# Kernel tuning notes

Measured on AMD Instinct MI355X. Metric: run time of the kernel, lower is better.

Reference implementation:

```python
import jax, jax.numpy as jnp
import numpy as np

B, N, F, K = 512, 512, 512, 10
D = F // 2

def setup_inputs() -> dict:
    key = jax.random.key(0)
    k1, k2, k3 = jax.random.split(key, 3)
    ins_emb = jax.random.normal(k1, (B, N, F), dtype=jnp.float32)
    attn = jax.random.uniform(k2, (B, N, 1), dtype=jnp.float32)
    # xavier_uniform for a (D, D) linear weight
    limit = float(np.sqrt(6.0 / (D + D)))
    W = jax.random.uniform(k3, (D, D), dtype=jnp.float32, minval=-limit, maxval=limit)
    return {"ins_emb": ins_emb, "attn": attn, "W": W}

def reference(ins_emb, attn, W):
    d = ins_emb.shape[-1] // 2
    drug = ins_emb[:, :, :d]          # [B, N, d]
    dis = ins_emb[:, :, d:]           # [B, N, d]
    # torch Linear: drug @ W^T, then per-instance dot with dis -> scalar
    proj = jnp.einsum('bnd,ed->bne', drug, W)          # [B, N, d]
    pred = jnp.sum(proj * dis, axis=-1, keepdims=True) # [B, N, 1]
    attn_pred = attn * pred                            # [B, N, 1]
    topk_vals, _ = jax.lax.top_k(attn_pred[:, :, 0], K)  # [B, K]
    return jnp.mean(topk_vals, axis=1, keepdims=True)    # [B, 1]
```

## Files before the change

### kernel.cpp

```cpp
#include <hip/hip_runtime.h>
#include <hip/hip_bf16.h>
#include <cstdint>

#define BB 512
#define NN 512
#define FF 512
#define DD 256
#define KTOP 10
#define BN (BB*NN)
#define BM 16
#define NTILES (BN/BM)
#define GRID 256
#define TPB (NTILES/GRID)

typedef __attribute__((ext_vector_type(8))) short bf16x8;
typedef __attribute__((ext_vector_type(4))) short s16x4;
typedef __attribute__((ext_vector_type(4))) float f32x4;

__device__ __forceinline__ ushort f2bf(float x){
  union { __hip_bfloat16 h; ushort u; } cv;
  cv.h = __float2bfloat16(x);
  return cv.u;
}

__device__ __forceinline__ bf16x8 cvt8(f32x4 a, f32x4 b){
  bf16x8 r;
  r[0]=(short)f2bf(a[0]); r[1]=(short)f2bf(a[1]); r[2]=(short)f2bf(a[2]); r[3]=(short)f2bf(a[3]);
  r[4]=(short)f2bf(b[0]); r[5]=(short)f2bf(b[1]); r[6]=(short)f2bf(b[2]); r[7]=(short)f2bf(b[3]);
  return r;
}

#define GL2LDS(GSRC, LDST)                                                          \
  __builtin_amdgcn_global_load_lds(                                                 \
      (const __attribute__((address_space(1))) uint32_t*)(uintptr_t)(GSRC),         \
      (__attribute__((address_space(3))) uint32_t*)(uint32_t)(uintptr_t)(LDST),     \
      16, 0, 0)

__global__ void wconv(const float* __restrict__ W, ushort* __restrict__ Wbf){
  int i = (blockIdx.x*256 + threadIdx.x)*4;
  float4 v = *reinterpret_cast<const float4*>(W + i);
  s16x4 o;
  o[0] = (short)f2bf(v.x); o[1] = (short)f2bf(v.y);
  o[2] = (short)f2bf(v.z); o[3] = (short)f2bf(v.w);
  *reinterpret_cast<s16x4*>(Wbf + i) = o;
}

__global__ __launch_bounds__(512, 2)
void score_kernel(const float* __restrict__ emb, const float* __restrict__ attn,
                  const ushort* __restrict__ Wbf, float* __restrict__ scores){
  __shared__ float Lbuf[4][BM*FF];
  __shared__ float red[2][8][BM];
  __shared__ float attn_l[TPB*BM];

  const int tid  = threadIdx.x;
  const int w    = tid >> 6;
  const int lane = tid & 63;
  const int g    = lane >> 4;
  const int c    = lane & 15;
  const int s    = w & 3;
  const int h    = w >> 2;

  attn_l[tid]       = attn[blockIdx.x*(TPB*BM) + tid];
  attn_l[tid + 512] = attn[blockIdx.x*(TPB*BM) + 512 + tid];

  bf16x8 Wf[4][4];
#pragma unroll
  for (int eb = 0; eb < 4; ++eb)
#pragma unroll
    for (int kb = 0; kb < 4; ++kb){
      int e = s*64 + eb*16 + c;
      int k = h*128 + kb*32 + g*8;
      Wf[eb][kb] = *reinterpret_cast<const bf16x8*>(Wbf + e*DD + k);
    }

  int offs[4];
#pragma unroll
  for (int i = 0; i < 4; ++i){
    int idx = w*4 + i;
    int r = idx >> 1, hf = idx & 1;
    offs[i] = r*FF + hf*256 + ((lane ^ (r & 7)) << 2);
  }
  const float* tbase = emb + (size_t)blockIdx.x * TPB * (BM*FF);

#pragma unroll
  for (int tt = 0; tt < 3; ++tt){
    const float* nb = tbase + (size_t)tt * (BM*FF);
#pragma unroll
    for (int i = 0; i < 4; ++i)
      GL2LDS(nb + offs[i], &Lbuf[tt][(w*4 + i)*256]);
  }

  for (int t = 0; t < TPB; ++t){
    if (t + 2 < TPB)      asm volatile("s_waitcnt vmcnt(8) lgkmcnt(0)" ::: "memory");
    else if (t + 1 < TPB) asm volatile("s_waitcnt vmcnt(4) lgkmcnt(0)" ::: "memory");
    else                  asm volatile("s_waitcnt vmcnt(0) lgkmcnt(0)" ::: "memory");
    __builtin_amdgcn_s_barrier();
    __builtin_amdgcn_sched_barrier(0);

    if (t + 3 < TPB){
      const float* nb = tbase + (size_t)(t+3) * (BM*FF);
#pragma unroll
      for (int i = 0; i < 4; ++i)
        GL2LDS(nb + offs[i], &Lbuf[(t+3) & 3][(w*4 + i)*256]);
    }

    if (t > 0 && tid < BM){
      const int tp = t - 1;
      float sum = red[tp&1][0][tid] + red[tp&1][1][tid] + red[tp&1][2][tid] + red[tp&1][3][tid]
                + red[tp&1][4][tid] + red[tp&1][5][tid] + red[tp&1][6][tid] + red[tp&1][7][tid];
      int row = (blockIdx.x*TPB + tp)*BM + tid;
      scores[row] = attn_l[tp*BM + tid] * sum;
    }

    const f32x4* Lv = (const f32x4*)&Lbuf[t & 3][0];
    const int rb = c*128;
    const int x  = c & 7;
    bf16x8 af[4];
#pragma unroll
    for (int kb = 0; kb < 4; ++kb){
      int ch0 = h*32 + kb*8 + g*2;
      f32x4 q0 = Lv[rb + ((ch0    ) ^ x)];
      f32x4 q1 = Lv[rb + ((ch0 + 1) ^ x)];
      af[kb] = cvt8(q0, q1);
    }
    float rs0=0.f, rs1=0.f, rs2=0.f, rs3=0.f;
#pragma unroll
    for (int eb = 0; eb < 4; ++eb){
      f32x4 acc = {0.f, 0.f, 0.f, 0.f};
#pragma unroll
      for (int kb = 0; kb < 4; ++kb)
        acc = __builtin_amdgcn_mfma_f32_16x16x32_bf16(af[kb], Wf[eb][kb], acc, 0, 0, 0);
      const int sb = 64 + s*16 + eb*4 + (c >> 2);
      const int e3 = c & 3;
#pragma unroll
      for (int j = 0; j < 4; ++j){
        const int row = g*4 + j;
        const int fi  = row*FF + ((sb ^ (row & 7)) << 2) + e3;
        float d = Lbuf[t & 3][fi];
        if      (j == 0) rs0 += acc[0]*d;
        else if (j == 1) rs1 += acc[1]*d;
        else if (j == 2) rs2 += acc[2]*d;
        else             rs3 += acc[3]*d;
      }
    }
    rs0 += __shfl_xor(rs0,1); rs0 += __shfl_xor(rs0,2); rs0 += __shfl_xor(rs0,4); rs0 += __shfl_xor(rs0,8);
    rs1 += __shfl_xor(rs1,1); rs1 += __shfl_xor(rs1,2); rs1 += __shfl_xor(rs1,4); rs1 += __shfl_xor(rs1,8);
    rs2 += __shfl_xor(rs2,1); rs2 += __shfl_xor(rs2,2); rs2 += __shfl_xor(rs2,4); rs2 += __shfl_xor(rs2,8);
    rs3 += __shfl_xor(rs3,1); rs3 += __shfl_xor(rs3,2); rs3 += __shfl_xor(rs3,4); rs3 += __shfl_xor(rs3,8);
    if (c == 0){
      red[t&1][w][g*4 + 0] = rs0;
      red[t&1][w][g*4 + 1] = rs1;
      red[t&1][w][g*4 + 2] = rs2;
      red[t&1][w][g*4 + 3] = rs3;
    }
  }

  asm volatile("s_waitcnt lgkmcnt(0)" ::: "memory");
  __builtin_amdgcn_s_barrier();
  if (tid < BM){
    const int tp = TPB - 1;
    float sum = red[tp&1][0][tid] + red[tp&1][1][tid] + red[tp&1][2][tid] + red[tp&1][3][tid]
              + red[tp&1][4][tid] + red[tp&1][5][tid] + red[tp&1][6][tid] + red[tp&1][7][tid];
    int row = (blockIdx.x*TPB + tp)*BM + tid;
    scores[row] = attn_l[tp*BM + tid] * sum;
  }
}

__global__ void topk_kernel(const float* __restrict__ scores, float* __restrict__ out){
  const int b = blockIdx.x;
  const int lane = threadIdx.x;
  float v0,v1,v2,v3,v4,v5,v6,v7;
  const float* sc = scores + b*NN;
  v0=sc[lane]; v1=sc[64+lane]; v2=sc[128+lane]; v3=sc[192+lane];
  v4=sc[256+lane]; v5=sc[320+lane]; v6=sc[384+lane]; v7=sc[448+lane];
  float total = 0.f;
  for (int it = 0; it < KTOP; ++it){
    float m = v0; int mj = 0;
    if (v1>m){m=v1;mj=1;} if (v2>m){m=v2;mj=2;} if (v3>m){m=v3;mj=3;}
    if (v4>m){m=v4;mj=4;} if (v5>m){m=v5;mj=5;} if (v6>m){m=v6;mj=6;}
    if (v7>m){m=v7;mj=7;}
    float bm = m; int bl = lane;
#pragma unroll
    for (int off = 32; off; off >>= 1){
      float om = __shfl_xor(bm, off);
      int   ol = __shfl_xor(bl, off);
      if (om > bm || (om == bm && ol < bl)){ bm = om; bl = ol; }
    }
    total += bm;
    if (lane == bl){
      if (mj==0) v0=-3.0e38f; else if (mj==1) v1=-3.0e38f;
      else if (mj==2) v2=-3.0e38f; else if (mj==3) v3=-3.0e38f;
      else if (mj==4) v4=-3.0e38f; else if (mj==5) v5=-3.0e38f;
      else if (mj==6) v6=-3.0e38f; else v7=-3.0e38f;
    }
  }
  if (lane == 0) out[b] = total * (1.0f / KTOP);
}

extern "C" void kernel_launch(void* const* d_in, const int* in_sizes, int n_in,
                              void* d_out, int out_size, void* d_ws, size_t ws_size,
                              hipStream_t stream){
  const float* emb  = (const float*)d_in[0];
  const float* attn = (const float*)d_in[1];
  const float* W    = (const float*)d_in[2];
  float* out = (float*)d_out;

  ushort* Wbf    = (ushort*)d_ws;
  float*  scores = (float*)((char*)d_ws + DD*DD*sizeof(ushort));

  wconv<<<64, 256, 0, stream>>>(W, Wbf);
  score_kernel<<<GRID, 512, 0, stream>>>(emb, attn, Wbf, scores);
  topk_kernel<<<BB, 64, 0, stream>>>(scores, out);
}
```

Before: 116.0 us.

## Fuse weight conversion, scoring and top-k into one per-batch kernel

Replaces the three-kernel pipeline (W bf16 conversion, tiled score kernel, top-k kernel) with a single kernel that runs one block per batch row. Each block converts fp32 W into bf16 fragments itself, keeps scores in LDS and does the top-10 mean at the end. This removes two launches and the global round trip for scores. In exchange the emb prefetch drops from a 4-stage to a 2-stage buffer with a full __syncthreads every tile, and every block re-reads the fp32 W. That may expose more memory latency in what is a bandwidth-bound stream.

```diff
diff --git a/kernel.cpp b/kernel.cpp
--- a/kernel.cpp
+++ b/kernel.cpp
@@ -7,14 +7,11 @@
 #define FF 512
 #define DD 256
 #define KTOP 10
-#define BN (BB*NN)
 #define BM 16
-#define NTILES (BN/BM)
-#define GRID 256
-#define TPB (NTILES/GRID)
+#define GRID 512
+#define TPB (NN/BM)
 
 typedef __attribute__((ext_vector_type(8))) short bf16x8;
-typedef __attribute__((ext_vector_type(4))) short s16x4;
 typedef __attribute__((ext_vector_type(4))) float f32x4;
 
 __device__ __forceinline__ ushort f2bf(float x){
@@ -36,22 +33,15 @@
       (__attribute__((address_space(3))) uint32_t*)(uint32_t)(uintptr_t)(LDST),     \
       16, 0, 0)
 
-__global__ void wconv(const float* __restrict__ W, ushort* __restrict__ Wbf){
-  int i = (blockIdx.x*256 + threadIdx.x)*4;
-  float4 v = *reinterpret_cast<const float4*>(W + i);
-  s16x4 o;
-  o[0] = (short)f2bf(v.x); o[1] = (short)f2bf(v.y);
-  o[2] = (short)f2bf(v.z); o[3] = (short)f2bf(v.w);
-  *reinterpret_cast<s16x4*>(Wbf + i) = o;
-}
+__global__ __launch_bounds__(512, 4)
+void fused_kernel(const float* __restrict__ emb, const float* __restrict__ attn,
+                  const float* __restrict__ W, float* __restrict__ out){
+  __shared__ float Lbuf[2][BM*FF];
+  __shared__ float red[2][8][BM];
+  __shared__ float attn_l[NN];
+  __shared__ float scores_l[NN];
 
-__global__ __launch_bounds__(512, 2)
-void score_kernel(const float* __restrict__ emb, const float* __restrict__ attn,
-                  const ushort* __restrict__ Wbf, float* __restrict__ scores){
-  __shared__ float Lbuf[4][BM*FF];
-  __shared__ float red[2][8][BM];
-  __shared__ float attn_l[TPB*BM];
-
+  const int b    = blockIdx.x;
   const int tid  = threadIdx.x;
   const int w    = tid >> 6;
   const int lane = tid & 63;
@@ -60,19 +50,6 @@
   const int s    = w & 3;
   const int h    = w >> 2;
 
-  attn_l[tid]       = attn[blockIdx.x*(TPB*BM) + tid];
-  attn_l[tid + 512] = attn[blockIdx.x*(TPB*BM) + 512 + tid];
-
-  bf16x8 Wf[4][4];
-#pragma unroll
-  for (int eb = 0; eb < 4; ++eb)
-#pragma unroll
-    for (int kb = 0; kb < 4; ++kb){
-      int e = s*64 + eb*16 + c;
-      int k = h*128 + kb*32 + g*8;
-      Wf[eb][kb] = *reinterpret_cast<const bf16x8*>(Wbf + e*DD + k);
-    }
-
   int offs[4];
 #pragma unroll
   for (int i = 0; i < 4; ++i){
@@ -80,39 +57,36 @@
     int r = idx >> 1, hf = idx & 1;
     offs[i] = r*FF + hf*256 + ((lane ^ (r & 7)) << 2);
   }
-  const float* tbase = emb + (size_t)blockIdx.x * TPB * (BM*FF);
+  const float* tbase = emb + (size_t)b * (NN*FF);
 
 #pragma unroll
-  for (int tt = 0; tt < 3; ++tt){
-    const float* nb = tbase + (size_t)tt * (BM*FF);
+  for (int i = 0; i < 4; ++i)
+    GL2LDS(tbase + offs[i], &Lbuf[0][(w*4 + i)*256]);
+
+  attn_l[tid] = attn[b*NN + tid];
+
+  bf16x8 Wf[4][4];
 #pragma unroll
-    for (int i = 0; i < 4; ++i)
-      GL2LDS(nb + offs[i], &Lbuf[tt][(w*4 + i)*256]);
-  }
+  for (int eb = 0; eb < 4; ++eb)
+#pragma unroll
+    for (int kb = 0; kb < 4; ++kb){
+      const float* wp = W + (s*64 + eb*16 + c)*DD + h*128 + kb*32 + g*8;
+      f32x4 q0 = *reinterpret_cast<const f32x4*>(wp);
+      f32x4 q1 = *reinterpret_cast<const f32x4*>(wp + 4);
+      Wf[eb][kb] = cvt8(q0, q1);
+    }
+
+  __syncthreads();
 
   for (int t = 0; t < TPB; ++t){
-    if (t + 2 < TPB)      asm volatile("s_waitcnt vmcnt(8) lgkmcnt(0)" ::: "memory");
-    else if (t + 1 < TPB) asm volatile("s_waitcnt vmcnt(4) lgkmcnt(0)" ::: "memory");
-    else                  asm volatile("s_waitcnt vmcnt(0) lgkmcnt(0)" ::: "memory");
-    __builtin_amdgcn_s_barrier();
-    __builtin_amdgcn_sched_barrier(0);
-
-    if (t + 3 < TPB){
-      const float* nb = tbase + (size_t)(t+3) * (BM*FF);
+    if (t + 1 < TPB){
+      const float* nb = tbase + (size_t)(t+1) * (BM*FF);
 #pragma unroll
       for (int i = 0; i < 4; ++i)
-        GL2LDS(nb + offs[i], &Lbuf[(t+3) & 3][(w*4 + i)*256]);
+        GL2LDS(nb + offs[i], &Lbuf[(t+1) & 1][(w*4 + i)*256]);
     }
 
-    if (t > 0 && tid < BM){
-      const int tp = t - 1;
-      float sum = red[tp&1][0][tid] + red[tp&1][1][tid] + red[tp&1][2][tid] + red[tp&1][3][tid]
-                + red[tp&1][4][tid] + red[tp&1][5][tid] + red[tp&1][6][tid] + red[tp&1][7][tid];
-      int row = (blockIdx.x*TPB + tp)*BM + tid;
-      scores[row] = attn_l[tp*BM + tid] * sum;
-    }
-
-    const f32x4* Lv = (const f32x4*)&Lbuf[t & 3][0];
+    const f32x4* Lv = (const f32x4*)&Lbuf[t & 1][0];
     const int rb = c*128;
     const int x  = c & 7;
     bf16x8 af[4];
@@ -136,7 +110,7 @@
       for (int j = 0; j < 4; ++j){
         const int row = g*4 + j;
         const int fi  = row*FF + ((sb ^ (row & 7)) << 2) + e3;
-        float d = Lbuf[t & 3][fi];
+        float d = Lbuf[t & 1][fi];
         if      (j == 0) rs0 += acc[0]*d;
         else if (j == 1) rs1 += acc[1]*d;
         else if (j == 2) rs2 += acc[2]*d;
@@ -153,48 +127,45 @@
       red[t&1][w][g*4 + 2] = rs2;
       red[t&1][w][g*4 + 3] = rs3;
     }
+
+    __syncthreads();
+
+    if (tid < BM){
+      float sum = red[t&1][0][tid] + red[t&1][1][tid] + red[t&1][2][tid] + red[t&1][3][tid]
+                + red[t&1][4][tid] + red[t&1][5][tid] + red[t&1][6][tid] + red[t&1][7][tid];
+      scores_l[t*BM + tid] = attn_l[t*BM + tid] * sum;
+    }
   }
 
-  asm volatile("s_waitcnt lgkmcnt(0)" ::: "memory");
-  __builtin_amdgcn_s_barrier();
-  if (tid < BM){
-    const int tp = TPB - 1;
-    float sum = red[tp&1][0][tid] + red[tp&1][1][tid] + red[tp&1][2][tid] + red[tp&1][3][tid]
-              + red[tp&1][4][tid] + red[tp&1][5][tid] + red[tp&1][6][tid] + red[tp&1][7][tid];
-    int row = (blockIdx.x*TPB + tp)*BM + tid;
-    scores[row] = attn_l[tp*BM + tid] * sum;
+  __syncthreads();
+
+  if (w == 0){
+    float v0,v1,v2,v3,v4,v5,v6,v7;
+    v0=scores_l[lane];     v1=scores_l[64+lane];  v2=scores_l[128+lane]; v3=scores_l[192+lane];
+    v4=scores_l[256+lane]; v5=scores_l[320+lane]; v6=scores_l[384+lane]; v7=scores_l[448+lane];
+    float total = 0.f;
+    for (int it = 0; it < KTOP; ++it){
+      float m = v0; int mj = 0;
+      if (v1>m){m=v1;mj=1;} if (v2>m){m=v2;mj=2;} if (v3>m){m=v3;mj=3;}
+      if (v4>m){m=v4;mj=4;} if (v5>m){m=v5;mj=5;} if (v6>m){m=v6;mj=6;}
+      if (v7>m){m=v7;mj=7;}
+      float bm = m; int bl = lane;
+#pragma unroll
+      for (int off = 32; off; off >>= 1){
+        float om = __shfl_xor(bm, off);
+        int   ol = __shfl_xor(bl, off);
+        if (om > bm || (om == bm && ol < bl)){ bm = om; bl = ol; }
+      }
+      total += bm;
+      if (lane == bl){
+        if (mj==0) v0=-3.0e38f; else if (mj==1) v1=-3.0e38f;
+        else if (mj==2) v2=-3.0e38f; else if (mj==3) v3=-3.0e38f;
+        else if (mj==4) v4=-3.0e38f; else if (mj==5) v5=-3.0e38f;
+        else if (mj==6) v6=-3.0e38f; else v7=-3.0e38f;
+      }
+    }
+    if (lane == 0) out[b] = total * (1.0f / KTOP);
   }
-}
-
-__global__ void topk_kernel(const float* __restrict__ scores, float* __restrict__ out){
-  const int b = blockIdx.x;
-  const int lane = threadIdx.x;
-  float v0,v1,v2,v3,v4,v5,v6,v7;
-  const float* sc = scores + b*NN;
-  v0=sc[lane]; v1=sc[64+lane]; v2=sc[128+lane]; v3=sc[192+lane];
-  v4=sc[256+lane]; v5=sc[320+lane]; v6=sc[384+lane]; v7=sc[448+lane];
-  float total = 0.f;
-  for (int it = 0; it < KTOP; ++it){
-    float m = v0; int mj = 0;
-    if (v1>m){m=v1;mj=1;} if (v2>m){m=v2;mj=2;} if (v3>m){m=v3;mj=3;}
-    if (v4>m){m=v4;mj=4;} if (v5>m){m=v5;mj=5;} if (v6>m){m=v6;mj=6;}
-    if (v7>m){m=v7;mj=7;}
-    float bm = m; int bl = lane;
-#pragma unroll
-    for (int off = 32; off; off >>= 1){
-      float om = __shfl_xor(bm, off);
-      int   ol = __shfl_xor(bl, off);
-      if (om > bm || (om == bm && ol < bl)){ bm = om; bl = ol; }
-    }
-    total += bm;
-    if (lane == bl){
-      if (mj==0) v0=-3.0e38f; else if (mj==1) v1=-3.0e38f;
-      else if (mj==2) v2=-3.0e38f; else if (mj==3) v3=-3.0e38f;
-      else if (mj==4) v4=-3.0e38f; else if (mj==5) v5=-3.0e38f;
-      else if (mj==6) v6=-3.0e38f; else v7=-3.0e38f;
-    }
-  }
-  if (lane == 0) out[b] = total * (1.0f / KTOP);
 }
 
 extern "C" void kernel_launch(void* const* d_in, const int* in_sizes, int n_in,
@@ -205,10 +176,5 @@
   const float* W    = (const float*)d_in[2];
   float* out = (float*)d_out;
 
-  ushort* Wbf    = (ushort*)d_ws;
-  float*  scores = (float*)((char*)d_ws + DD*DD*sizeof(ushort));
-
-  wconv<<<64, 256, 0, stream>>>(W, Wbf);
-  score_kernel<<<GRID, 512, 0, stream>>>(emb, attn, Wbf, scores);
-  topk_kernel<<<BB, 64, 0, stream>>>(scores, out);
+  fused_kernel<<<GRID, 512, 0, stream>>>(emb, attn, W, out);
 }
```

New measurement: 185.6 us. 1.6x slower.
